# Kernel tuning notes

Hardware: AMD Instinct MI355X
Metric: run time of the kernel (lower is better)

The kernel has to match this reference:

```python
import jax, jax.numpy as jnp
import numpy as np

ROPE_BASE = 10000.0

def _rope(x, positions):
    # x: (B, h, T, d); standard half-split rotary embedding with d_key = d
    d = x.shape[-1]
    inv_freq = 1.0 / (ROPE_BASE ** (jnp.arange(0, d // 2, dtype=jnp.float32) / (d // 2)))
    ang = positions.astype(jnp.float32)[:, None] * inv_freq[None, :]  # (T, d/2)
    cos, sin = jnp.cos(ang), jnp.sin(ang)
    x1, x2 = x[..., : d // 2], x[..., d // 2 :]
    return jnp.concatenate([x1 * cos - x2 * sin, x1 * sin + x2 * cos], axis=-1)


def setup_inputs() -> dict:
    key = jax.random.key(0)
    k1, k2, k3 = jax.random.split(key, 3)
    B, T, d, h = 2, 2048, 768, 8
    std = d ** -0.5
    x = jax.random.normal(k1, (B, T, d), dtype=jnp.float32)
    M = jax.random.normal(k2, (d, h * d), dtype=jnp.float32) * std
    V = jax.random.normal(k3, (d, h * d), dtype=jnp.float32) * std
    positions = jnp.arange(T, dtype=jnp.int32)
    return {"x": x, "M": M, "V": V, "positions": positions}


def reference(x, M, V, positions):
    B, T, d = x.shape
    h = M.shape[1] // d
    scale = 1.0 / jnp.sqrt(jnp.float32(d))
    # Q = RoPE(X @ M), K = RoPE(X) broadcast across heads, val = X @ V
    Q = (x @ M).reshape(B, T, h, d).transpose(0, 2, 1, 3)   # (B,h,T,d)
    val = (x @ V).reshape(B, T, h, d).transpose(0, 2, 1, 3)  # (B,h,T,d)
    K = jnp.broadcast_to(x[:, None, :, :], (B, h, T, d))     # (B,h,T,d)
    Q = _rope(Q, positions)
    K = _rope(K, positions)
    scores = jnp.einsum("bhqd,bhkd->bhqk", Q, K) * scale     # (B,h,T,T)
    causal = jnp.tril(jnp.ones((T, T), dtype=bool))          # True = keep
    scores = jnp.where(causal[None, None], scores, -jnp.inf)
    attn = jax.nn.softmax(scores, axis=-1)
    out = jnp.einsum("bhqk,bhkd->bhqd", attn, val)
    return out.sum(axis=1)  # sum over heads -> (B,T,d)
```

## Files before the change

### kernel.cpp

```cpp
#include <hip/hip_runtime.h>
#include <hip/hip_bf16.h>

typedef __bf16 bf16x8 __attribute__((ext_vector_type(8)));
typedef float f32x4 __attribute__((ext_vector_type(4)));
typedef float f32x16 __attribute__((ext_vector_type(16)));

#define SCALE 0.03608439182435161f
#define NEGINF (-1e30f)

static __device__ __forceinline__ ushort f2bf(float f) {
    union { float f; unsigned u; } v; v.f = f;
    unsigned r = (v.u + 0x7fff + ((v.u >> 16) & 1)) >> 16;
    return (ushort)r;
}
static __device__ __forceinline__ float bf2f(ushort u) {
    union { unsigned u; float f; } v; v.u = ((unsigned)u) << 16;
    return v.f;
}

static __device__ __forceinline__ void gload16(const void* g, void* lds) {
    __builtin_amdgcn_global_load_lds((const __attribute__((address_space(1))) void*)g,
                                     (__attribute__((address_space(3))) void*)lds, 16, 0, 0);
}

#define PHASEB do { asm volatile("s_waitcnt vmcnt(0) lgkmcnt(0)" ::: "memory"); \
                    __builtin_amdgcn_s_barrier(); \
                    asm volatile("" ::: "memory"); } while (0)
#define BARL do { asm volatile("s_waitcnt lgkmcnt(0)" ::: "memory"); \
                  __builtin_amdgcn_s_barrier(); \
                  asm volatile("" ::: "memory"); } while (0)

__global__ void k_convx(const float* __restrict__ x, ushort* __restrict__ xb, int n4) {
    int i = blockIdx.x * blockDim.x + threadIdx.x;
    if (i >= n4) return;
    float4 v = ((const float4*)x)[i];
    ushort4 o; o.x = f2bf(v.x); o.y = f2bf(v.y); o.z = f2bf(v.z); o.w = f2bf(v.w);
    ((ushort4*)xb)[i] = o;
}

__global__ void k_tconv(const float* __restrict__ in, ushort* __restrict__ out, int R, int C) {
    __shared__ float ts[32][33];
    int r0 = blockIdx.x * 32, c0 = blockIdx.y * 32;
    int lr = threadIdx.x >> 5, lc = threadIdx.x & 31;
#pragma unroll
    for (int i = 0; i < 4; i++) ts[lr + i * 8][lc] = in[(r0 + lr + i * 8) * C + c0 + lc];
    __syncthreads();
#pragma unroll
    for (int i = 0; i < 4; i++) out[(c0 + lr + i * 8) * R + r0 + lc] = f2bf(ts[lc][lr + i * 8]);
}

template <int EPI>
__global__ __launch_bounds__(256) void k_gemm(const ushort* __restrict__ A,
                                              const ushort* __restrict__ Bt,
                                              ushort* __restrict__ out) {
    __shared__ ushort As[128 * 32];
    __shared__ ushort Bs[128 * 32];
    const int m0 = blockIdx.x * 128, n0 = blockIdx.y * 128;
    const int tid = threadIdx.x, lane = tid & 63, wid = tid >> 6;
    const int wm = (wid >> 1) * 64, wn = (wid & 1) * 64;
    const int l15 = lane & 15, l4 = lane >> 4;
    const int srow = tid >> 2, scol = (tid & 3) * 8;
    f32x4 acc[4][4] = {};

    for (int kt = 0; kt < 768; kt += 32) {
        gload16(&A[(size_t)(m0 + srow) * 768 + kt + scol],       (char*)As + wid * 1024);
        gload16(&A[(size_t)(m0 + 64 + srow) * 768 + kt + scol],  (char*)As + 4096 + wid * 1024);
        gload16(&Bt[(size_t)(n0 + srow) * 768 + kt + scol],      (char*)Bs + wid * 1024);
        gload16(&Bt[(size_t)(n0 + 64 + srow) * 768 + kt + scol], (char*)Bs + 4096 + wid * 1024);
        PHASEB;
        bf16x8 af[4], bfr[4];
#pragma unroll
        for (int m = 0; m < 4; m++)
            af[m] = *(const bf16x8*)&As[(wm + m * 16 + l15) * 32 + l4 * 8];
#pragma unroll
        for (int n = 0; n < 4; n++)
            bfr[n] = *(const bf16x8*)&Bs[(wn + n * 16 + l15) * 32 + l4 * 8];
#pragma unroll
        for (int m = 0; m < 4; m++)
#pragma unroll
            for (int n = 0; n < 4; n++)
                acc[m][n] = __builtin_amdgcn_mfma_f32_16x16x32_bf16(af[m], bfr[n], acc[m][n], 0, 0, 0);
        BARL;
    }

#pragma unroll
    for (int m = 0; m < 4; m++) {
#pragma unroll
        for (int n = 0; n < 4; n++) {
#pragma unroll
            for (int r = 0; r < 4; r++) {
                int row = m0 + wm + m * 16 + (lane >> 4) * 4 + r;
                int col = n0 + wn + n * 16 + (lane & 15);
                float v = acc[m][n][r];
                int idx;
                if (EPI == 0) {
                    int b = row >> 11, t = row & 2047;
                    int hh = col / 768, dd = col - hh * 768;
                    idx = ((b * 8 + hh) * 2048 + t) * 768 + dd;
                } else {
                    int hh = row / 768, dd = row - hh * 768;
                    int b = col >> 11, t = col & 2047;
                    idx = ((b * 8 + hh) * 768 + dd) * 2048 + t;
                }
                out[idx] = f2bf(v);
            }
        }
    }
}

__global__ void k_ropeq(ushort* __restrict__ Q, const int* __restrict__ pos, int nrows) {
    int i = blockIdx.x * blockDim.x + threadIdx.x;
    int row = i / 96, j4 = (i % 96) * 4;
    if (row >= nrows) return;
    float p = (float)pos[row & 2047];
    ushort4 u1 = *(ushort4*)&Q[row * 768 + j4];
    ushort4 u2 = *(ushort4*)&Q[row * 768 + 384 + j4];
    ushort4 o1, o2;
#pragma unroll
    for (int k = 0; k < 4; k++) {
        float inv = exp2f(-(float)(j4 + k) * (13.287712379549449f / 384.0f));
        float ang = p * inv;
        float s, c; sincosf(ang, &s, &c);
        float x1 = bf2f(((ushort*)&u1)[k]), x2 = bf2f(((ushort*)&u2)[k]);
        ((ushort*)&o1)[k] = f2bf((x1 * c - x2 * s) * SCALE);
        ((ushort*)&o2)[k] = f2bf((x1 * s + x2 * c) * SCALE);
    }
    *(ushort4*)&Q[row * 768 + j4] = o1;
    *(ushort4*)&Q[row * 768 + 384 + j4] = o2;
}

__global__ void k_ropek(const float* __restrict__ x, ushort* __restrict__ Kr,
                        const int* __restrict__ pos, int nrows) {
    int i = blockIdx.x * blockDim.x + threadIdx.x;
    int row = i / 96, j4 = (i % 96) * 4;
    if (row >= nrows) return;
    float p = (float)pos[row & 2047];
    float4 x1 = *(const float4*)&x[row * 768 + j4];
    float4 x2 = *(const float4*)&x[row * 768 + 384 + j4];
    ushort4 o1, o2;
    float a1[4] = {x1.x, x1.y, x1.z, x1.w};
    float a2[4] = {x2.x, x2.y, x2.z, x2.w};
#pragma unroll
    for (int k = 0; k < 4; k++) {
        float inv = exp2f(-(float)(j4 + k) * (13.287712379549449f / 384.0f));
        float ang = p * inv;
        float s, c; sincosf(ang, &s, &c);
        ((ushort*)&o1)[k] = f2bf(a1[k] * c - a2[k] * s);
        ((ushort*)&o2)[k] = f2bf(a1[k] * s + a2[k] * c);
    }
    *(ushort4*)&Kr[row * 768 + j4] = o1;
    *(ushort4*)&Kr[row * 768 + 384 + j4] = o2;
}

__global__ __launch_bounds__(512, 2) void k_attn(const ushort* Qr, const ushort* __restrict__ Kr,
                                                 const ushort* __restrict__ valT, ushort* Oh) {
    __shared__ alignas(128) char Qs[98304];
    __shared__ alignas(128) char pool[65536];

    const int p = blockIdx.x, hh = blockIdx.y, b = blockIdx.z;
    const int bh = b * 8 + hh;
    const int tid = threadIdx.x, lane = tid & 63, wid = tid >> 6;
    const int g = wid & 3, qh = wid >> 2;
    const int l31 = lane & 31, hi = lane >> 5;
    const int hi16 = hi << 4;

    const int row0 = tid >> 4, col16 = tid & 15;
    const int swz = (col16 << 4) ^ ((row0 & 15) << 4);

    const int arow = g * 32 + l31;
    const int qrow = qh * 32 + l31;
    const int asw = (arow & 15) << 4;
    const int qsw = (qrow & 15) << 4;

    char* Pb = pool + 32768;
    float* pmax_s = (float*)(pool + 49152);
    float* psum_s = (float*)(pool + 50176);
    float* stat_s = (float*)(pool + 51200);

    const char* Kb0 = (const char*)Kr + ((size_t)(b * 2048 + row0)) * 1536 + swz;
    const char* Vb0 = (const char*)valT + ((size_t)(bh * 768 + row0)) * 4096 + swz;

    for (int ti = 0; ti < 2; ti++) {
        const int qt = ti ? (31 - p) : p;
        const int q0 = qt * 64;
        const int nkb = (qt + 2) >> 1;
        const int qg = q0 + qrow;

        const char* qsrc = (const char*)Qr + ((size_t)(bh * 2048 + q0 + row0)) * 1536 + swz;
#pragma unroll
        for (int r = 0; r < 12; r++)
            gload16(qsrc + (r >> 1) * 256 + (size_t)(r & 1) * 49152,
                    Qs + (r >> 1) * 16384 + (r & 1) * 8192 + wid * 1024);
#pragma unroll
        for (int r = 0; r < 4; r++)
            gload16(Kb0 + (size_t)r * 49152, pool + r * 8192 + wid * 1024);

        float m_r = NEGINF, l_r = 0.f;
        f32x16 oacc[6] = {};

        for (int kb = 0; kb < nkb; kb++) {
            const char* kc = Kb0 + (size_t)kb * 196608;
            const char* vc = Vb0 + (size_t)kb * 256;
            const bool nx = (kb + 1 < nkb);
            const bool nm = (kb * 128 + 127 > q0);

            f32x16 sacc = {};
#pragma unroll
            for (int c = 0; c < 6; c++) {
                PHASEB;
                if (c < 5) {
#pragma unroll
                    for (int r = 0; r < 4; r++)
                        gload16(kc + (c + 1) * 256 + (size_t)r * 49152,
                                pool + ((c + 1) & 1) * 32768 + r * 8192 + wid * 1024);
                } else {
#pragma unroll
                    for (int r = 0; r < 4; r++)
                        gload16(vc + (size_t)r * 131072, pool + r * 8192 + wid * 1024);
                }
                const char* kbuf = pool + (c & 1) * 32768;
                const char* qcb = Qs + c * 16384;
                __builtin_amdgcn_s_setprio(1);
#pragma unroll
                for (int s = 0; s < 8; s++) {
                    bf16x8 a = *(const bf16x8*)(kbuf + arow * 256 + ((s * 32 + hi16) ^ asw));
                    bf16x8 bq = *(const bf16x8*)(qcb + qrow * 256 + ((s * 32 + hi16) ^ qsw));
                    sacc = __builtin_amdgcn_mfma_f32_32x32x16_bf16(a, bq, sacc, 0, 0, 0);
                }
                __builtin_amdgcn_s_setprio(0);
            }

            BARL;

            const int kbase_ = kb * 128 + g * 32 + 4 * hi;
            float mloc = NEGINF;
            if (nm) {
#pragma unroll
                for (int r = 0; r < 16; r++) {
                    int kg = kbase_ + (r & 3) + 8 * (r >> 2);
                    float v = (kg > qg) ? NEGINF : sacc[r];
                    mloc = fmaxf(mloc, v);
                }
            } else {
#pragma unroll
                for (int r = 0; r < 16; r++) mloc = fmaxf(mloc, sacc[r]);
            }
            mloc = fmaxf(mloc, __shfl_xor(mloc, 32));
            if (hi == 0) pmax_s[qrow * 4 + g] = mloc;
            BARL;

            float4 pm = *(const float4*)&pmax_s[qrow * 4];
            float m_new = fmaxf(fmaxf(fmaxf(pm.x, pm.y), fmaxf(pm.z, pm.w)), m_r);
            float rv = __expf(m_r - m_new);
            float ps = 0.f; uint w[8];
            if (nm) {
#pragma unroll
                for (int j = 0; j < 8; j++) {
                    int kg0 = kbase_ + ((2 * j) & 3) + 8 * ((2 * j) >> 2);
                    int kg1 = kbase_ + ((2 * j + 1) & 3) + 8 * ((2 * j + 1) >> 2);
                    float e0 = (kg0 > qg) ? 0.f : __expf(sacc[2 * j] - m_new);
                    float e1 = (kg1 > qg) ? 0.f : __expf(sacc[2 * j + 1] - m_new);
                    ps += e0 + e1;
                    w[j] = (uint)f2bf(e0) | ((uint)f2bf(e1) << 16);
                }
            } else {
#pragma unroll
                for (int j = 0; j < 8; j++) {
                    float e0 = __expf(sacc[2 * j] - m_new);
                    float e1 = __expf(sacc[2 * j + 1] - m_new);
                    ps += e0 + e1;
                    w[j] = (uint)f2bf(e0) | ((uint)f2bf(e1) << 16);
                }
            }
            ps += __shfl_xor(ps, 32);
            if (hi == 0) psum_s[qrow * 4 + g] = ps;
            if (g == 0 && hi == 0) stat_s[qrow] = rv;
#pragma unroll
            for (int j = 0; j < 4; j++) {
                uint2 pw; pw.x = w[2 * j]; pw.y = w[2 * j + 1];
                *(uint2*)(Pb + qrow * 256 + ((g * 64 + j * 16 + hi * 8) ^ qsw)) = pw;
            }
            BARL;

            float4 ps4 = *(const float4*)&psum_s[qrow * 4];
            l_r = l_r * rv + (ps4.x + ps4.y + ps4.z + ps4.w);
            m_r = m_new;
            float rs[16];
#pragma unroll
            for (int r = 0; r < 16; r++)
                rs[r] = stat_s[qh * 32 + (r & 3) + 8 * (r >> 2) + 4 * hi];
#pragma unroll
            for (int c = 0; c < 6; c++)
#pragma unroll
                for (int r = 0; r < 16; r++) oacc[c][r] *= rs[r];
            bf16x8 pa[8];
#pragma unroll
            for (int s = 0; s < 8; s++)
                pa[s] = *(const bf16x8*)(Pb + qrow * 256 + ((s * 32 + hi16) ^ qsw));

#pragma unroll
            for (int c = 0; c < 6; c++) {
                PHASEB;
                if (c < 5) {
#pragma unroll
                    for (int r = 0; r < 4; r++)
                        gload16(vc + (size_t)(c + 1) * 524288 + (size_t)r * 131072,
                                pool + ((c + 1) & 1) * 32768 + r * 8192 + wid * 1024);
                } else if (nx) {
#pragma unroll
                    for (int r = 0; r < 4; r++)
                        gload16(kc + 196608 + (size_t)r * 49152, pool + r * 8192 + wid * 1024);
                }
                const char* vbuf = pool + (c & 1) * 32768;
                __builtin_amdgcn_s_setprio(1);
#pragma unroll
                for (int s = 0; s < 8; s++) {
                    bf16x8 bv = *(const bf16x8*)(vbuf + arow * 256 + ((s * 32 + hi16) ^ asw));
                    oacc[c] = __builtin_amdgcn_mfma_f32_32x32x16_bf16(pa[s], bv, oacc[c], 0, 0, 0);
                }
                __builtin_amdgcn_s_setprio(0);
            }
        }

        BARL;
        if (g == 0 && hi == 0) stat_s[qrow] = l_r;
        BARL;
        float inv16[16];
#pragma unroll
        for (int r = 0; r < 16; r++)
            inv16[r] = 1.0f / stat_s[qh * 32 + (r & 3) + 8 * (r >> 2) + 4 * hi];
        BARL;
        ushort* obase = Oh + ((size_t)(bh * 2048 + q0 + qh * 32)) * 768;
#pragma unroll
        for (int c = 0; c < 6; c++) {
            int dd = c * 128 + g * 32 + l31;
#pragma unroll
            for (int r = 0; r < 16; r++) {
                int rq = (r & 3) + 8 * (r >> 2) + 4 * hi;
                obase[(size_t)rq * 768 + dd] = f2bf(oacc[c][r] * inv16[r]);
            }
        }
    }
}

__global__ void k_reduce(const ushort* __restrict__ Oh, float* __restrict__ out) {
    int i = blockIdx.x * blockDim.x + threadIdx.x;
    if (i >= 786432) return;
    size_t base = (size_t)i * 4;
    int b = (base >= 1572864) ? 1 : 0;
    size_t rem = base - (size_t)b * 1572864;
    const ushort* src = Oh + (size_t)b * 8 * 1572864 + rem;
    float4 acc = {0.f, 0.f, 0.f, 0.f};
#pragma unroll
    for (int h = 0; h < 8; h++) {
        ushort4 v = *(const ushort4*)(src + (size_t)h * 1572864);
        acc.x += bf2f(v.x); acc.y += bf2f(v.y); acc.z += bf2f(v.z); acc.w += bf2f(v.w);
    }
    *(float4*)&out[base] = acc;
}

extern "C" void kernel_launch(void* const* d_in, const int* in_sizes, int n_in,
                              void* d_out, int out_size, void* d_ws, size_t ws_size,
                              hipStream_t stream) {
    const float* x = (const float*)d_in[0];
    const float* M = (const float*)d_in[1];
    const float* V = (const float*)d_in[2];
    const int* pos = (const int*)d_in[3];
    float* out = (float*)d_out;
    char* ws = (char*)d_ws;

    ushort* xb   = (ushort*)(ws);
    ushort* Mt   = (ushort*)(ws + 6291456);
    ushort* Vt   = (ushort*)(ws + 15728640);
    ushort* Qr   = (ushort*)(ws + 25165824);
    ushort* valT = (ushort*)(ws + 75497472);
    ushort* Kr   = (ushort*)(ws + 125829120);

    k_convx<<<3072, 256, 0, stream>>>(x, xb, 786432);
    k_tconv<<<dim3(24, 192), 256, 0, stream>>>(M, Mt, 768, 6144);
    k_tconv<<<dim3(24, 192), 256, 0, stream>>>(V, Vt, 768, 6144);
    k_gemm<0><<<dim3(32, 48), 256, 0, stream>>>(xb, Mt, Qr);
    k_gemm<1><<<dim3(48, 32), 256, 0, stream>>>(Vt, xb, valT);
    k_ropeq<<<12288, 256, 0, stream>>>(Qr, pos, 32768);
    k_ropek<<<1536, 256, 0, stream>>>(x, Kr, pos, 4096);
    k_attn<<<dim3(16, 8, 2), 512, 0, stream>>>(Qr, Kr, valT, Qr );
    k_reduce<<<3072, 256, 0, stream>>>(Qr, out);
}
```

Measured before the change: 359.7 us.

## Fuse Q RoPE into attention and merge softmax max/sum into one barrier

Removes the standalone Q RoPE kernel and applies the rotation to the Q tile in shared memory right after it is loaded inside the attention kernel, so Q no longer makes a separate read-modify-write pass through global memory. The softmax statistics are restructured: each wave computes a local max and local exp-sum together and publishes them as one float2. This drops one shared-memory exchange and the extra rescale-factor broadcast, which now uses lane shuffles. The final normalisation also reads l_r via shuffles instead of extra barriers. The cost is extra exp work per tile for the local sums and fast-math sincos for the in-kernel RoPE.

After: 354.4 us. No clear change (-1.5%).

```diff
diff --git a/kernel.cpp b/kernel.cpp
--- a/kernel.cpp
+++ b/kernel.cpp
@@ -108,27 +108,6 @@
     }
 }
 
-__global__ void k_ropeq(ushort* __restrict__ Q, const int* __restrict__ pos, int nrows) {
-    int i = blockIdx.x * blockDim.x + threadIdx.x;
-    int row = i / 96, j4 = (i % 96) * 4;
-    if (row >= nrows) return;
-    float p = (float)pos[row & 2047];
-    ushort4 u1 = *(ushort4*)&Q[row * 768 + j4];
-    ushort4 u2 = *(ushort4*)&Q[row * 768 + 384 + j4];
-    ushort4 o1, o2;
-#pragma unroll
-    for (int k = 0; k < 4; k++) {
-        float inv = exp2f(-(float)(j4 + k) * (13.287712379549449f / 384.0f));
-        float ang = p * inv;
-        float s, c; sincosf(ang, &s, &c);
-        float x1 = bf2f(((ushort*)&u1)[k]), x2 = bf2f(((ushort*)&u2)[k]);
-        ((ushort*)&o1)[k] = f2bf((x1 * c - x2 * s) * SCALE);
-        ((ushort*)&o2)[k] = f2bf((x1 * s + x2 * c) * SCALE);
-    }
-    *(ushort4*)&Q[row * 768 + j4] = o1;
-    *(ushort4*)&Q[row * 768 + 384 + j4] = o2;
-}
-
 __global__ void k_ropek(const float* __restrict__ x, ushort* __restrict__ Kr,
                         const int* __restrict__ pos, int nrows) {
     int i = blockIdx.x * blockDim.x + threadIdx.x;
@@ -153,7 +132,8 @@
 }
 
 __global__ __launch_bounds__(512, 2) void k_attn(const ushort* Qr, const ushort* __restrict__ Kr,
-                                                 const ushort* __restrict__ valT, ushort* Oh) {
+                                                 const ushort* __restrict__ valT,
+                                                 const int* __restrict__ pos, ushort* Oh) {
     __shared__ alignas(128) char Qs[98304];
     __shared__ alignas(128) char pool[65536];
 
@@ -173,9 +153,7 @@
     const int qsw = (qrow & 15) << 4;
 
     char* Pb = pool + 32768;
-    float* pmax_s = (float*)(pool + 49152);
-    float* psum_s = (float*)(pool + 50176);
-    float* stat_s = (float*)(pool + 51200);
+    float2* stats = (float2*)(pool + 49152);
 
     const char* Kb0 = (const char*)Kr + ((size_t)(b * 2048 + row0)) * 1536 + swz;
     const char* Vb0 = (const char*)valT + ((size_t)(bh * 768 + row0)) * 4096 + swz;
@@ -195,6 +173,40 @@
         for (int r = 0; r < 4; r++)
             gload16(Kb0 + (size_t)r * 49152, pool + r * 8192 + wid * 1024);
 
+        PHASEB;
+
+        {
+            const int rr = tid >> 3;
+            const int gb0 = (tid & 7) * 16;
+            const int rsw = (rr & 15) << 4;
+            const float pf = (float)pos[q0 + rr];
+#pragma unroll
+            for (int c = 0; c < 3; c++) {
+#pragma unroll
+                for (int h2 = 0; h2 < 2; h2++) {
+                    int gb = gb0 + h2 * 128;
+                    char* p1 = Qs + c * 16384 + rr * 256 + (gb ^ rsw);
+                    char* p2 = Qs + (c + 3) * 16384 + rr * 256 + (gb ^ rsw);
+                    uint4 u1 = *(uint4*)p1, u2 = *(uint4*)p2;
+                    uint4 o1, o2;
+                    ushort* a1 = (ushort*)&u1; ushort* a2 = (ushort*)&u2;
+                    ushort* b1 = (ushort*)&o1; ushort* b2 = (ushort*)&o2;
+#pragma unroll
+                    for (int k = 0; k < 8; k++) {
+                        float dv = (float)(c * 128 + (gb >> 1) + k);
+                        float inv = exp2f(-dv * (13.287712379549449f / 384.0f));
+                        float ang = pf * inv;
+                        float sn, cs; __sincosf(ang, &sn, &cs);
+                        float x1 = bf2f(a1[k]), x2 = bf2f(a2[k]);
+                        b1[k] = f2bf((x1 * cs - x2 * sn) * SCALE);
+                        b2[k] = f2bf((x1 * sn + x2 * cs) * SCALE);
+                    }
+                    *(uint4*)p1 = o1; *(uint4*)p2 = o2;
+                }
+            }
+        }
+        BARL;
+
         float m_r = NEGINF, l_r = 0.f;
         f32x16 oacc[6] = {};
 
@@ -233,26 +245,38 @@
             BARL;
 
             const int kbase_ = kb * 128 + g * 32 + 4 * hi;
-            float mloc = NEGINF;
+            float mloc = NEGINF, sloc = 0.f;
             if (nm) {
 #pragma unroll
                 for (int r = 0; r < 16; r++) {
                     int kg = kbase_ + (r & 3) + 8 * (r >> 2);
-                    float v = (kg > qg) ? NEGINF : sacc[r];
-                    mloc = fmaxf(mloc, v);
+                    if (kg <= qg) mloc = fmaxf(mloc, sacc[r]);
+                }
+                mloc = fmaxf(mloc, __shfl_xor(mloc, 32));
+#pragma unroll
+                for (int r = 0; r < 16; r++) {
+                    int kg = kbase_ + (r & 3) + 8 * (r >> 2);
+                    sloc += (kg <= qg) ? __expf(sacc[r] - mloc) : 0.f;
                 }
             } else {
 #pragma unroll
                 for (int r = 0; r < 16; r++) mloc = fmaxf(mloc, sacc[r]);
-            }
-            mloc = fmaxf(mloc, __shfl_xor(mloc, 32));
-            if (hi == 0) pmax_s[qrow * 4 + g] = mloc;
+                mloc = fmaxf(mloc, __shfl_xor(mloc, 32));
+#pragma unroll
+                for (int r = 0; r < 16; r++) sloc += __expf(sacc[r] - mloc);
+            }
+            sloc += __shfl_xor(sloc, 32);
+            if (hi == 0) stats[qrow * 4 + g] = make_float2(mloc, sloc);
             BARL;
 
-            float4 pm = *(const float4*)&pmax_s[qrow * 4];
-            float m_new = fmaxf(fmaxf(fmaxf(pm.x, pm.y), fmaxf(pm.z, pm.w)), m_r);
+            float4 sa = *(const float4*)(stats + qrow * 4);
+            float4 sb = *(const float4*)(stats + qrow * 4 + 2);
+            float m_new = fmaxf(fmaxf(fmaxf(sa.x, sa.z), fmaxf(sb.x, sb.z)), m_r);
             float rv = __expf(m_r - m_new);
-            float ps = 0.f; uint w[8];
+            float lad = sa.y * __expf(sa.x - m_new) + sa.w * __expf(sa.z - m_new)
+                      + sb.y * __expf(sb.x - m_new) + sb.w * __expf(sb.z - m_new);
+            l_r = l_r * rv + lad; m_r = m_new;
+            uint w[8];
             if (nm) {
 #pragma unroll
                 for (int j = 0; j < 8; j++) {
@@ -260,7 +284,6 @@
                     int kg1 = kbase_ + ((2 * j + 1) & 3) + 8 * ((2 * j + 1) >> 2);
                     float e0 = (kg0 > qg) ? 0.f : __expf(sacc[2 * j] - m_new);
                     float e1 = (kg1 > qg) ? 0.f : __expf(sacc[2 * j + 1] - m_new);
-                    ps += e0 + e1;
                     w[j] = (uint)f2bf(e0) | ((uint)f2bf(e1) << 16);
                 }
             } else {
@@ -268,13 +291,9 @@
                 for (int j = 0; j < 8; j++) {
                     float e0 = __expf(sacc[2 * j] - m_new);
                     float e1 = __expf(sacc[2 * j + 1] - m_new);
-                    ps += e0 + e1;
                     w[j] = (uint)f2bf(e0) | ((uint)f2bf(e1) << 16);
                 }
             }
-            ps += __shfl_xor(ps, 32);
-            if (hi == 0) psum_s[qrow * 4 + g] = ps;
-            if (g == 0 && hi == 0) stat_s[qrow] = rv;
 #pragma unroll
             for (int j = 0; j < 4; j++) {
                 uint2 pw; pw.x = w[2 * j]; pw.y = w[2 * j + 1];
@@ -282,13 +301,10 @@
             }
             BARL;
 
-            float4 ps4 = *(const float4*)&psum_s[qrow * 4];
-            l_r = l_r * rv + (ps4.x + ps4.y + ps4.z + ps4.w);
-            m_r = m_new;
             float rs[16];
 #pragma unroll
             for (int r = 0; r < 16; r++)
-                rs[r] = stat_s[qh * 32 + (r & 3) + 8 * (r >> 2) + 4 * hi];
+                rs[r] = __shfl(rv, (r & 3) + 8 * (r >> 2) + 4 * hi);
 #pragma unroll
             for (int c = 0; c < 6; c++)
 #pragma unroll
@@ -322,14 +338,10 @@
             }
         }
 
-        BARL;
-        if (g == 0 && hi == 0) stat_s[qrow] = l_r;
-        BARL;
         float inv16[16];
 #pragma unroll
         for (int r = 0; r < 16; r++)
-            inv16[r] = 1.0f / stat_s[qh * 32 + (r & 3) + 8 * (r >> 2) + 4 * hi];
-        BARL;
+            inv16[r] = 1.0f / __shfl(l_r, (r & 3) + 8 * (r >> 2) + 4 * hi);
         ushort* obase = Oh + ((size_t)(bh * 2048 + q0 + qh * 32)) * 768;
 #pragma unroll
         for (int c = 0; c < 6; c++) {
@@ -381,8 +393,7 @@
     k_tconv<<<dim3(24, 192), 256, 0, stream>>>(V, Vt, 768, 6144);
     k_gemm<0><<<dim3(32, 48), 256, 0, stream>>>(xb, Mt, Qr);
     k_gemm<1><<<dim3(48, 32), 256, 0, stream>>>(Vt, xb, valT);
-    k_ropeq<<<12288, 256, 0, stream>>>(Qr, pos, 32768);
     k_ropek<<<1536, 256, 0, stream>>>(x, Kr, pos, 4096);
-    k_attn<<<dim3(16, 8, 2), 512, 0, stream>>>(Qr, Kr, valT, Qr );
+    k_attn<<<dim3(16, 8, 2), 512, 0, stream>>>(Qr, Kr, valT, pos, Qr );
     k_reduce<<<3072, 256, 0, stream>>>(Qr, out);
 }
```
